# Optimization experiments

Measured on AMD Instinct MI355X. Metric: run time of the kernel, lower is better.

## Reference

```python
import jax, jax.numpy as jnp
import numpy as np

N = 10000        # num_nodes
E = 160000       # num_edges (before self loops)
D_IN = 256       # input_dim
H = 128          # hidden_dim (= per-head out_channels)
HEADS = 4
HD = HEADS * H   # 512
L = 16           # num_layers
OUT = 1024       # output_dim
G = 8            # num graphs in batch
EPS = 1e-5


def _layer_norm(x, w, b):
    m = jnp.mean(x, axis=-1, keepdims=True)
    v = jnp.mean(jnp.square(x - m), axis=-1, keepdims=True)
    return (x - m) / jnp.sqrt(v + EPS) * w + b


def setup_inputs() -> dict:
    key = jax.random.key(0)
    ks = jax.random.split(key, 20)
    s = 0.05
    x = jax.random.normal(ks[0], (N, D_IN), jnp.float32)
    edge_index = jax.random.randint(ks[1], (2, E), 0, N, dtype=jnp.int64)
    batch = jnp.sort(jax.random.randint(ks[2], (N,), 0, G, dtype=jnp.int64))
    return {
        "x": x,
        "edge_index": edge_index,
        "batch": batch,
        "W_in": jax.random.normal(ks[3], (D_IN, H), jnp.float32) * s,
        "b_in": jnp.zeros((H,), jnp.float32),
        "ln_in_w": jnp.ones((H,), jnp.float32),
        "ln_in_b": jnp.zeros((H,), jnp.float32),
        "Wsrc": jax.random.normal(ks[4], (L, H, HD), jnp.float32) * s,
        "Wdst": jax.random.normal(ks[5], (L, H, HD), jnp.float32) * s,
        "att_src": jax.random.normal(ks[6], (L, HEADS, H), jnp.float32) * s,
        "att_dst": jax.random.normal(ks[7], (L, HEADS, H), jnp.float32) * s,
        "Wout": jax.random.normal(ks[8], (L, HD, H), jnp.float32) * s,
        "bout": jnp.zeros((L, H), jnp.float32),
        "ln_w": jnp.ones((L, H), jnp.float32),
        "ln_b": jnp.zeros((L, H), jnp.float32),
        "Wp1": jax.random.normal(ks[9], (H, OUT), jnp.float32) * s,
        "bp1": jnp.zeros((OUT,), jnp.float32),
        "Wp2": jax.random.normal(ks[10], (OUT, OUT), jnp.float32) * s,
        "bp2": jnp.zeros((OUT,), jnp.float32),
    }


def reference(x, edge_index, batch, W_in, b_in, ln_in_w, ln_in_b,
              Wsrc, Wdst, att_src, att_dst, Wout, bout, ln_w, ln_b,
              Wp1, bp1, Wp2, bp2):
    # add self loops once (same edge set every layer)
    loop = jnp.arange(N, dtype=edge_index.dtype)
    e_src = jnp.concatenate([edge_index[0], loop])  # x_j (source)
    e_dst = jnp.concatenate([edge_index[1], loop])  # x_i (target / aggregate index)

    h = jax.nn.relu(_layer_norm(x @ W_in + b_in, ln_in_w, ln_in_b))  # [N, H]

    for l in range(L):
        hs = (h[e_src] @ Wsrc[l]).reshape(-1, HEADS, H)  # [E2, heads, H]
        hd = (h[e_dst] @ Wdst[l]).reshape(-1, HEADS, H)
        a = jnp.sum(hs * att_src[l], axis=-1) + jnp.sum(hd * att_dst[l], axis=-1)  # [E2, heads]
        a = jax.nn.leaky_relu(a, 0.2)
        # NOTE: faithful to source -- softmax over HEADS per edge, not over neighbors
        a = jax.nn.softmax(a, axis=-1)
        msg = (hs * a[..., None]).reshape(-1, HD)  # [E2, HD]
        agg = jax.ops.segment_sum(msg, e_dst, num_segments=N)  # [N, HD]
        out = agg @ Wout[l] + bout[l]
        h = jax.nn.relu(_layer_norm(out + h, ln_w[l], ln_b[l]))  # residual: H == H

    g = jax.ops.segment_max(h, batch, num_segments=G)  # global max pool [G, H]
    g = jax.nn.relu(g @ Wp1 + bp1)
    return g @ Wp2 + bp2  # [G, OUT]
```

## Files before the change

### kernel.cpp

```cpp
#include <hip/hip_runtime.h>
#include <hip/hip_bf16.h>

#define N_NODES 10000
#define E_EDGES 160000
#define E2 (E_EDGES + N_NODES)
#define D_IN 256
#define H 128
#define HEADS 4
#define HD 512
#define L_LAYERS 16
#define OUT_DIM 1024
#define G_GRAPHS 8
#define EPS 1e-5f
#define SPAD 10016

typedef unsigned short ushort_t;
typedef __attribute__((ext_vector_type(8))) short short8;
typedef __attribute__((ext_vector_type(4))) float f32x4;
typedef __attribute__((ext_vector_type(4))) unsigned u32x4;

__device__ __forceinline__ f32x4 mfma16(short8 a, short8 b, f32x4 c) {
    return __builtin_amdgcn_mfma_f32_16x16x32_bf16(a, b, c, 0, 0, 0);
}
__device__ __forceinline__ unsigned short f2b(float f) {
    unsigned u = __float_as_uint(f);
    u += 0x7fffu + ((u >> 16) & 1u);
    return (unsigned short)(u >> 16);
}
__device__ __forceinline__ unsigned pk2(float lo, float hi) {
    __hip_bfloat162 p = __float22bfloat162_rn(make_float2(lo, hi));
    return *(unsigned*)&p;
}

__global__ void k_zero(int* deg, int* cur, unsigned* g) {
    int i = blockIdx.x * blockDim.x + threadIdx.x;
    if (i < N_NODES) { deg[i] = 0; cur[i] = 0; }
    if (i < G_GRAPHS * H) g[i] = 0u;
}

__global__ void k_count(const int* ei, int* deg) {
    int e = blockIdx.x * blockDim.x + threadIdx.x;
    if (e >= E2) return;
    int d = (e < E_EDGES) ? ei[E_EDGES + e] : (e - E_EDGES);
    atomicAdd(&deg[d], 1);
}

__global__ void k_scan(const int* deg, int* rs) {
    __shared__ int s[1024];
    int t = threadIdx.x;
    int base = t * 10;
    int loc[10], run = 0;
    #pragma unroll
    for (int i = 0; i < 10; i++) {
        int idx = base + i;
        int v = (idx < N_NODES) ? deg[idx] : 0;
        loc[i] = run; run += v;
    }
    s[t] = run;
    __syncthreads();
    for (int off = 1; off < 1024; off <<= 1) {
        int xv = (t >= off) ? s[t - off] : 0;
        __syncthreads();
        s[t] += xv;
        __syncthreads();
    }
    int excl = s[t] - run;
    #pragma unroll
    for (int i = 0; i < 10; i++) {
        int idx = base + i;
        if (idx <= N_NODES) rs[idx] = excl + loc[i];
    }
}

__global__ void k_fill(const int* ei, const int* rs, int* cur, int* elist) {
    int e = blockIdx.x * blockDim.x + threadIdx.x;
    if (e >= E2) return;
    int s, d;
    if (e < E_EDGES) { s = ei[e]; d = ei[E_EDGES + e]; }
    else { s = d = e - E_EDGES; }
    int pos = atomicAdd(&cur[d], 1);
    elist[rs[d] + pos] = s;
}

__global__ void k_vw(const float* Wsrc, const float* Wdst,
                     const float* att_src, const float* att_dst,
                     float* vsrc, float* vdst) {
    int l = blockIdx.x;
    int t = threadIdx.x;
    int head = t >> 7, j = t & 127;
    const float* Ws = Wsrc + (size_t)l * H * HD;
    const float* Wd = Wdst + (size_t)l * H * HD;
    const float* As = att_src + (size_t)l * HEADS * H;
    const float* Ad = att_dst + (size_t)l * HEADS * H;
    float ss = 0.f, sd = 0.f;
    for (int k = 0; k < H; k++) {
        ss += Ws[(size_t)j * HD + head * H + k] * As[head * H + k];
        sd += Wd[(size_t)j * HD + head * H + k] * Ad[head * H + k];
    }
    vsrc[(size_t)l * HD + head * H + j] = ss;
    vdst[(size_t)l * HD + head * H + j] = sd;
}

__global__ __launch_bounds__(256) void k_mm(const float* __restrict__ Wsrc,
        const float* __restrict__ Wout, float* __restrict__ M) {
    int bid = blockIdx.x;
    int kq = bid & 3, h = (bid >> 2) & 3, l = bid >> 4;
    int t = threadIdx.x;
    int o = t & 127, kh = t >> 7;
    const float* Ws = Wsrc + (size_t)l * H * HD + h * 128;
    const float* Wo = Wout + (size_t)l * HD * H + (size_t)h * 128 * H;
    for (int r = 0; r < 16; r++) {
        int k = kq * 32 + kh * 16 + r;
        float acc = 0.f;
        for (int c = 0; c < 128; c++)
            acc += Ws[(size_t)k * HD + c] * Wo[(size_t)c * H + o];
        M[(size_t)l * HD * H + (size_t)(h * 128 + k) * H + o] = acc;
    }
}

__global__ void k_pack_out(const float* W, ushort_t* Wp) {
    int idx = blockIdx.x * 256 + threadIdx.x;
    int l = idx >> 16, rem = idx & 65535;
    int k = rem >> 7, col = rem & 127;
    float v = W[(size_t)l * HD * H + (size_t)k * H + col];
    int nt = col >> 4, ks = k >> 5, lhi = (k >> 3) & 3, llo = col & 15, j = k & 7;
    Wp[(size_t)l * 65536 + (((size_t)(nt * 16 + ks) * 64) + lhi * 16 + llo) * 8 + j] = f2b(v);
}

__global__ void k_pack_win(const float* W, ushort_t* Wp) {
    int idx = blockIdx.x * 256 + threadIdx.x;
    int k = idx >> 7, col = idx & 127;
    float v = W[(size_t)k * H + col];
    int nt = col >> 4, ks = k >> 5, lhi = (k >> 3) & 3, llo = col & 15, j = k & 7;
    Wp[(((size_t)(nt * 8 + ks) * 64) + lhi * 16 + llo) * 8 + j] = f2b(v);
}

__global__ __launch_bounds__(256) void k_in_mfma(
        const float* __restrict__ x, const ushort_t* __restrict__ WpI,
        const float* __restrict__ b_in, const float* __restrict__ lnw,
        const float* __restrict__ lnb, float* __restrict__ h, ushort_t* __restrict__ hb) {
    __shared__ float part1[4][16], part2[4][16];
    int t = threadIdx.x, w = t >> 6, lane = t & 63;
    int row0 = blockIdx.x * 16;
    int ar = lane & 15, ac = (lane >> 4) * 8;
    short8 a[8];
    #pragma unroll
    for (int ks = 0; ks < 8; ks++) {
        const float* xp = x + (size_t)(row0 + ar) * D_IN + ks * 32 + ac;
        float4 xa = *(const float4*)xp;
        float4 xb = *(const float4*)(xp + 4);
        u32x4 u;
        u.x = pk2(xa.x, xa.y); u.y = pk2(xa.z, xa.w);
        u.z = pk2(xb.x, xb.y); u.w = pk2(xb.z, xb.w);
        a[ks] = *(short8*)&u;
    }
    const ushort_t* B0 = WpI + ((size_t)(w * 2 + 0) * 8) * 64 * 8;
    const ushort_t* B1 = WpI + ((size_t)(w * 2 + 1) * 8) * 64 * 8;
    f32x4 c0 = {0.f, 0.f, 0.f, 0.f}, c1 = {0.f, 0.f, 0.f, 0.f};
    #pragma unroll
    for (int ks = 0; ks < 8; ks++) {
        short8 b0 = *(const short8*)(B0 + ((size_t)ks * 64 + lane) * 8);
        short8 b1 = *(const short8*)(B1 + ((size_t)ks * 64 + lane) * 8);
        c0 = mfma16(a[ks], b0, c0);
        c1 = mfma16(a[ks], b1, c1);
    }
    int col0 = (w * 2 + 0) * 16 + ar, col1 = (w * 2 + 1) * 16 + ar;
    int rb = (lane >> 4) * 4;
    float v0[4], v1[4];
    #pragma unroll
    for (int r = 0; r < 4; r++) {
        v0[r] = c0[r] + b_in[col0];
        v1[r] = c1[r] + b_in[col1];
        float p1 = v0[r] + v1[r];
        float p2 = v0[r] * v0[r] + v1[r] * v1[r];
        #pragma unroll
        for (int off = 1; off < 16; off <<= 1) {
            p1 += __shfl_xor(p1, off);
            p2 += __shfl_xor(p2, off);
        }
        if (ar == 0) { part1[w][rb + r] = p1; part2[w][rb + r] = p2; }
    }
    __syncthreads();
    #pragma unroll
    for (int r = 0; r < 4; r++) {
        int lr = rb + r;
        int row = row0 + lr;
        float s1 = part1[0][lr] + part1[1][lr] + part1[2][lr] + part1[3][lr];
        float s2 = part2[0][lr] + part2[1][lr] + part2[2][lr] + part2[3][lr];
        float m = s1 * (1.f / 128.f);
        float var = s2 * (1.f / 128.f) - m * m;
        float is = rsqrtf(var + EPS);
        float y0 = fmaxf((v0[r] - m) * is * lnw[col0] + lnb[col0], 0.f);
        float y1 = fmaxf((v1[r] - m) * is * lnw[col1] + lnb[col1], 0.f);
        h[(size_t)row * H + col0] = y0;
        h[(size_t)row * H + col1] = y1;
        hb[(size_t)row * H + col0] = f2b(y0);
        hb[(size_t)row * H + col1] = f2b(y1);
    }
}

__global__ __launch_bounds__(256) void k_alpha(const float* __restrict__ h,
        const float* __restrict__ vsrc, const float* __restrict__ vdst,
        float* __restrict__ as_, float* __restrict__ ad_, int l) {
    int wid = threadIdx.x >> 6, lane = threadIdx.x & 63;
    int n = blockIdx.x * 4 + wid;
    float h0 = h[(size_t)n * H + lane];
    float h1 = h[(size_t)n * H + 64 + lane];
    const float* vs = vsrc + (size_t)l * HD;
    const float* vd = vdst + (size_t)l * HD;
    #pragma unroll
    for (int d = 0; d < HEADS; d++) {
        float p = h0 * vs[d * H + lane] + h1 * vs[d * H + 64 + lane];
        float q = h0 * vd[d * H + lane] + h1 * vd[d * H + 64 + lane];
        #pragma unroll
        for (int off = 32; off > 0; off >>= 1) {
            p += __shfl_down(p, off);
            q += __shfl_down(q, off);
        }
        if (lane == 0) { as_[n * HEADS + d] = p; ad_[n * HEADS + d] = q; }
    }
}

#define ACC1(uv, wt) do { \
    acc[0] += (wt) * __uint_as_float((uv).x << 16); \
    acc[1] += (wt) * __uint_as_float((uv).x & 0xffff0000u); \
    acc[2] += (wt) * __uint_as_float((uv).y << 16); \
    acc[3] += (wt) * __uint_as_float((uv).y & 0xffff0000u); \
    acc[4] += (wt) * __uint_as_float((uv).z << 16); \
    acc[5] += (wt) * __uint_as_float((uv).z & 0xffff0000u); \
    acc[6] += (wt) * __uint_as_float((uv).w << 16); \
    acc[7] += (wt) * __uint_as_float((uv).w & 0xffff0000u); \
} while (0)

__global__ __launch_bounds__(256) void k_aggout(
        const ushort_t* __restrict__ hb, const float4* __restrict__ as4,
        const float4* __restrict__ ad4, const int* __restrict__ rs,
        const int* __restrict__ elist, const ushort_t* __restrict__ Wp,
        const float* __restrict__ bout, const float* __restrict__ lnw,
        const float* __restrict__ lnb, float* __restrict__ h,
        ushort_t* __restrict__ hbo, int l) {
    __shared__ ushort_t frag[16 * 64 * 8];
    __shared__ int sl[4][64];
    __shared__ float wl[4][64][4];
    __shared__ float part1[4][16], part2[4][16];
    int t = threadIdx.x, w = t >> 6, lane = t & 63;
    int base = blockIdx.x * 16;
    int head = lane >> 4;
    int j8 = (lane & 15) * 8;

    for (int q = 0; q < 4; q++) {
        int r = w * 4 + q;
        int node = base + r;
        int start = rs[node], end = rs[node + 1];
        float4 adv = ad4[node];
        float acc[8];
        #pragma unroll
        for (int i = 0; i < 8; i++) acc[i] = 0.f;
        for (int c0 = start; c0 < end; c0 += 64) {
            int cnt = min(64, end - c0);
            if (lane < cnt) {
                int s = elist[c0 + lane];
                sl[w][lane] = s;
                float4 av = as4[s];
                float l0 = av.x + adv.x, l1 = av.y + adv.y, l2 = av.z + adv.z, l3 = av.w + adv.w;
                l0 = (l0 > 0.f) ? l0 : 0.2f * l0;
                l1 = (l1 > 0.f) ? l1 : 0.2f * l1;
                l2 = (l2 > 0.f) ? l2 : 0.2f * l2;
                l3 = (l3 > 0.f) ? l3 : 0.2f * l3;
                float mx = fmaxf(fmaxf(l0, l1), fmaxf(l2, l3));
                float e0 = expf(l0 - mx), e1 = expf(l1 - mx), e2 = expf(l2 - mx), e3 = expf(l3 - mx);
                float inv = 1.f / (e0 + e1 + e2 + e3);
                wl[w][lane][0] = e0 * inv;
                wl[w][lane][1] = e1 * inv;
                wl[w][lane][2] = e2 * inv;
                wl[w][lane][3] = e3 * inv;
            }
            __asm__ volatile("s_waitcnt lgkmcnt(0)" ::: "memory");
            int j = 0;
            if (cnt >= 4) {
                u32x4 b0, b1, b2, b3;
                float q0, q1, q2, q3;
                {
                    int s0 = sl[w][0], s1 = sl[w][1], s2 = sl[w][2], s3 = sl[w][3];
                    q0 = wl[w][0][head]; q1 = wl[w][1][head];
                    q2 = wl[w][2][head]; q3 = wl[w][3][head];
                    b0 = *(const u32x4*)(hb + (size_t)s0 * H + j8);
                    b1 = *(const u32x4*)(hb + (size_t)s1 * H + j8);
                    b2 = *(const u32x4*)(hb + (size_t)s2 * H + j8);
                    b3 = *(const u32x4*)(hb + (size_t)s3 * H + j8);
                }
                for (j = 4; j + 3 < cnt; j += 4) {
                    int s0 = sl[w][j], s1 = sl[w][j + 1], s2 = sl[w][j + 2], s3 = sl[w][j + 3];
                    u32x4 n0 = *(const u32x4*)(hb + (size_t)s0 * H + j8);
                    u32x4 n1 = *(const u32x4*)(hb + (size_t)s1 * H + j8);
                    u32x4 n2 = *(const u32x4*)(hb + (size_t)s2 * H + j8);
                    u32x4 n3 = *(const u32x4*)(hb + (size_t)s3 * H + j8);
                    float r0 = wl[w][j][head], r1 = wl[w][j + 1][head];
                    float r2 = wl[w][j + 2][head], r3 = wl[w][j + 3][head];
                    ACC1(b0, q0); ACC1(b1, q1); ACC1(b2, q2); ACC1(b3, q3);
                    b0 = n0; q0 = r0; b1 = n1; q1 = r1;
                    b2 = n2; q2 = r2; b3 = n3; q3 = r3;
                }
                ACC1(b0, q0); ACC1(b1, q1); ACC1(b2, q2); ACC1(b3, q3);
            }
            for (; j < cnt; j++) {
                int s = sl[w][j];
                float wt = wl[w][j][head];
                u32x4 uv = *(const u32x4*)(hb + (size_t)s * H + j8);
                ACC1(uv, wt);
            }
        }
        u32x4 o;
        o.x = pk2(acc[0], acc[1]);
        o.y = pk2(acc[2], acc[3]);
        o.z = pk2(acc[4], acc[5]);
        o.w = pk2(acc[6], acc[7]);
        int ksn = head * 4 + ((lane >> 2) & 3);
        int gidx = ((lane & 3) * 16 + r) * 16 + (ksn ^ r);
        *(u32x4*)((char*)frag + gidx * 16) = o;
    }
    __syncthreads();

    const ushort_t* WL = Wp + (size_t)l * 65536;
    short8 a[16];
    #pragma unroll
    for (int ks = 0; ks < 16; ks++) {
        int gidx = lane * 16 + (ks ^ (lane & 15));
        a[ks] = *(const short8*)((const char*)frag + gidx * 16);
    }
    int ar = lane & 15;
    f32x4 c0 = {0.f, 0.f, 0.f, 0.f}, c1 = {0.f, 0.f, 0.f, 0.f};
    #pragma unroll
    for (int ks = 0; ks < 16; ks++) {
        short8 b0 = *(const short8*)(WL + ((size_t)((w * 2 + 0) * 16 + ks) * 64 + lane) * 8);
        short8 b1 = *(const short8*)(WL + ((size_t)((w * 2 + 1) * 16 + ks) * 64 + lane) * 8);
        c0 = mfma16(a[ks], b0, c0);
        c1 = mfma16(a[ks], b1, c1);
    }

    const float* bo = bout + (size_t)l * H;
    const float* gw = lnw + (size_t)l * H;
    const float* gb = lnb + (size_t)l * H;
    int col0 = (w * 2 + 0) * 16 + ar;
    int col1 = (w * 2 + 1) * 16 + ar;
    int rb = (lane >> 4) * 4;
    float v0[4], v1[4];
    #pragma unroll
    for (int r = 0; r < 4; r++) {
        int row = base + rb + r;
        v0[r] = c0[r] + bo[col0] + h[(size_t)row * H + col0];
        v1[r] = c1[r] + bo[col1] + h[(size_t)row * H + col1];
        float p1 = v0[r] + v1[r];
        float p2 = v0[r] * v0[r] + v1[r] * v1[r];
        #pragma unroll
        for (int off = 1; off < 16; off <<= 1) {
            p1 += __shfl_xor(p1, off);
            p2 += __shfl_xor(p2, off);
        }
        if (ar == 0) { part1[w][rb + r] = p1; part2[w][rb + r] = p2; }
    }
    __syncthreads();
    #pragma unroll
    for (int r = 0; r < 4; r++) {
        int lr = rb + r;
        int row = base + lr;
        float s1 = part1[0][lr] + part1[1][lr] + part1[2][lr] + part1[3][lr];
        float s2 = part2[0][lr] + part2[1][lr] + part2[2][lr] + part2[3][lr];
        float m = s1 * (1.f / 128.f);
        float var = s2 * (1.f / 128.f) - m * m;
        float is = rsqrtf(var + EPS);
        float y0 = fmaxf((v0[r] - m) * is * gw[col0] + gb[col0], 0.f);
        float y1 = fmaxf((v1[r] - m) * is * gw[col1] + gb[col1], 0.f);
        h[(size_t)row * H + col0] = y0;
        h[(size_t)row * H + col1] = y1;
        hbo[(size_t)row * H + col0] = f2b(y0);
        hbo[(size_t)row * H + col1] = f2b(y1);
    }
}

__global__ void k_pool(const float* __restrict__ h, const int* __restrict__ batch,
                       unsigned* __restrict__ g) {
    __shared__ float lm[G_GRAPHS][H];
    int t = threadIdx.x;
    #pragma unroll
    for (int i = 0; i < G_GRAPHS; i++) lm[i][t] = 0.f;
    int n0 = blockIdx.x * 100, n1 = n0 + 100;
    for (int n = n0; n < n1; n++) {
        int b = batch[n];
        lm[b][t] = fmaxf(lm[b][t], h[(size_t)n * H + t]);
    }
    #pragma unroll
    for (int i = 0; i < G_GRAPHS; i++)
        atomicMax(&g[i * H + t], __float_as_uint(lm[i][t]));
}

__global__ void k_mlp1(const unsigned* __restrict__ g, const float* __restrict__ Wp1,
                       const float* __restrict__ bp1, float* __restrict__ g1) {
    __shared__ float gs[H];
    int gr = blockIdx.x >> 2, ch = blockIdx.x & 3;
    int t = threadIdx.x;
    if (t < H) gs[t] = __uint_as_float(g[gr * H + t]);
    __syncthreads();
    int col = ch * 256 + t;
    float acc = 0.f;
    for (int k = 0; k < H; k++) acc += gs[k] * Wp1[(size_t)k * OUT_DIM + col];
    acc += bp1[col];
    g1[(size_t)gr * OUT_DIM + col] = fmaxf(acc, 0.f);
}

__global__ void k_mlp2(const float* __restrict__ g1, const float* __restrict__ Wp2,
                       const float* __restrict__ bp2, float* __restrict__ out) {
    __shared__ float gs[OUT_DIM];
    __shared__ float part[4][64];
    int gr = blockIdx.x >> 4, ch = blockIdx.x & 15;
    int t = threadIdx.x;
    int ci = t & 63, si = t >> 6;
    for (int i = t; i < OUT_DIM; i += 256) gs[i] = g1[(size_t)gr * OUT_DIM + i];
    __syncthreads();
    int col = ch * 64 + ci;
    float acc = 0.f;
    for (int k = si * 256; k < si * 256 + 256; k++)
        acc += gs[k] * Wp2[(size_t)k * OUT_DIM + col];
    part[si][ci] = acc;
    __syncthreads();
    if (si == 0) {
        float r = part[0][ci] + part[1][ci] + part[2][ci] + part[3][ci] + bp2[col];
        out[(size_t)gr * OUT_DIM + col] = r;
    }
}

extern "C" void kernel_launch(void* const* d_in, const int* in_sizes, int n_in,
                              void* d_out, int out_size, void* d_ws, size_t ws_size,
                              hipStream_t stream) {
    const float* x       = (const float*)d_in[0];
    const int*   ei      = (const int*)d_in[1];
    const int*   batch   = (const int*)d_in[2];
    const float* W_in    = (const float*)d_in[3];
    const float* b_in    = (const float*)d_in[4];
    const float* ln_in_w = (const float*)d_in[5];
    const float* ln_in_b = (const float*)d_in[6];
    const float* Wsrc    = (const float*)d_in[7];
    const float* Wdst    = (const float*)d_in[8];
    const float* att_src = (const float*)d_in[9];
    const float* att_dst = (const float*)d_in[10];
    const float* Wout    = (const float*)d_in[11];
    const float* bout    = (const float*)d_in[12];
    const float* ln_w    = (const float*)d_in[13];
    const float* ln_b    = (const float*)d_in[14];
    const float* Wp1     = (const float*)d_in[15];
    const float* bp1     = (const float*)d_in[16];
    const float* Wp2     = (const float*)d_in[17];
    const float* bp2     = (const float*)d_in[18];

    char* w = (char*)d_ws;
    auto alloc = [&](size_t bytes) { void* p = w; w += (bytes + 255) & ~(size_t)255; return p; };
    float*     h     = (float*)alloc((size_t)N_NODES * H * 4);
    ushort_t*  hb    = (ushort_t*)alloc((size_t)SPAD * H * 2);
    float*     as_   = (float*)alloc((size_t)SPAD * HEADS * 4);
    float*     ad_   = (float*)alloc((size_t)SPAD * HEADS * 4);
    float*     vsrc  = (float*)alloc((size_t)L_LAYERS * HD * 4);
    float*     vdst  = (float*)alloc((size_t)L_LAYERS * HD * 4);
    float*     M     = (float*)alloc((size_t)L_LAYERS * HD * H * 4);
    ushort_t*  WpM   = (ushort_t*)alloc((size_t)L_LAYERS * 65536 * 2);
    ushort_t*  WpI   = (ushort_t*)alloc((size_t)D_IN * H * 2);
    int*       deg   = (int*)alloc((size_t)N_NODES * 4);
    int*       rs    = (int*)alloc((size_t)(N_NODES + 1) * 4);
    int*       cur   = (int*)alloc((size_t)N_NODES * 4);
    int*       elist = (int*)alloc((size_t)E2 * 4);
    unsigned*  g     = (unsigned*)alloc((size_t)G_GRAPHS * H * 4);
    float*     g1    = (float*)alloc((size_t)G_GRAPHS * OUT_DIM * 4);

    k_zero<<<40, 256, 0, stream>>>(deg, cur, g);
    k_count<<<(E2 + 255) / 256, 256, 0, stream>>>(ei, deg);
    k_scan<<<1, 1024, 0, stream>>>(deg, rs);
    k_fill<<<(E2 + 255) / 256, 256, 0, stream>>>(ei, rs, cur, elist);
    k_vw<<<L_LAYERS, 512, 0, stream>>>(Wsrc, Wdst, att_src, att_dst, vsrc, vdst);
    k_mm<<<256, 256, 0, stream>>>(Wsrc, Wout, M);
    k_pack_out<<<4096, 256, 0, stream>>>(M, WpM);
    k_pack_win<<<128, 256, 0, stream>>>(W_in, WpI);
    k_in_mfma<<<N_NODES / 16, 256, 0, stream>>>(x, WpI, b_in, ln_in_w, ln_in_b, h, hb);

    for (int l = 0; l < L_LAYERS; l++) {
        k_alpha<<<N_NODES / 4, 256, 0, stream>>>(h, vsrc, vdst, as_, ad_, l);
        k_aggout<<<N_NODES / 16, 256, 0, stream>>>(hb, (const float4*)as_, (const float4*)ad_,
                                                   rs, elist, WpM, bout, ln_w, ln_b, h, hb, l);
    }

    k_pool<<<100, 128, 0, stream>>>(h, batch, g);
    k_mlp1<<<G_GRAPHS * 4, 256, 0, stream>>>(g, Wp1, bp1, g1);
    k_mlp2<<<G_GRAPHS * 16, 256, 0, stream>>>(g1, Wp2, bp2, (float*)d_out);
}
```

Measured before the change: 719.8 us.

## Fuse attention-logit computation into layer epilogue, split weights hi/lo, widen aggout

Removes the per-layer k_alpha launch by computing next-layer source/destination attention dot products inside the k_aggout epilogue (and the first layer's inside k_in_mfma), with ping-pong buffers for hb and alpha to avoid read/write races. The fused weight matrix is now stored as bf16 high plus bf16 residual parts and applied with twice the MFMAs for better precision. k_aggout moves to 512 threads with one 16-column tile per wave, and the weight-product precompute kernel uses shared-memory tiling. This saves sixteen launches and a read of h per layer, at the cost of extra MFMA work and a larger block.

```diff
diff --git a/kernel.cpp b/kernel.cpp
--- a/kernel.cpp
+++ b/kernel.cpp
@@ -26,6 +26,9 @@
     unsigned u = __float_as_uint(f);
     u += 0x7fffu + ((u >> 16) & 1u);
     return (unsigned short)(u >> 16);
+}
+__device__ __forceinline__ float b2f(unsigned short b) {
+    return __uint_as_float((unsigned)b << 16);
 }
 __device__ __forceinline__ unsigned pk2(float lo, float hi) {
     __hip_bfloat162 p = __float22bfloat162_rn(make_float2(lo, hi));
@@ -103,28 +106,68 @@
 
 __global__ __launch_bounds__(256) void k_mm(const float* __restrict__ Wsrc,
         const float* __restrict__ Wout, float* __restrict__ M) {
+    __shared__ float As[32][33];
+    __shared__ float Bs[32][128];
     int bid = blockIdx.x;
-    int kq = bid & 3, h = (bid >> 2) & 3, l = bid >> 4;
+    int q = bid & 3, hh = (bid >> 2) & 3, l = bid >> 4;
     int t = threadIdx.x;
-    int o = t & 127, kh = t >> 7;
-    const float* Ws = Wsrc + (size_t)l * H * HD + h * 128;
-    const float* Wo = Wout + (size_t)l * HD * H + (size_t)h * 128 * H;
-    for (int r = 0; r < 16; r++) {
-        int k = kq * 32 + kh * 16 + r;
-        float acc = 0.f;
-        for (int c = 0; c < 128; c++)
-            acc += Ws[(size_t)k * HD + c] * Wo[(size_t)c * H + o];
-        M[(size_t)l * HD * H + (size_t)(h * 128 + k) * H + o] = acc;
-    }
-}
-
-__global__ void k_pack_out(const float* W, ushort_t* Wp) {
+    int ty = t >> 4, tx = t & 15;
+    const float* WsB = Wsrc + (size_t)l * H * HD + (size_t)hh * 128;
+    const float* WoB = Wout + (size_t)l * HD * H + (size_t)hh * 128 * H;
+    float acc[2][8];
+    #pragma unroll
+    for (int r = 0; r < 2; r++)
+        #pragma unroll
+        for (int c = 0; c < 8; c++) acc[r][c] = 0.f;
+    for (int kt = 0; kt < 4; kt++) {
+        #pragma unroll
+        for (int i = 0; i < 4; i++) {
+            int lin = i * 256 + t;
+            int rr = lin >> 5, cc = lin & 31;
+            As[rr][cc] = WsB[(size_t)(q * 32 + rr) * HD + kt * 32 + cc];
+        }
+        #pragma unroll
+        for (int i = 0; i < 16; i++) {
+            int lin = i * 256 + t;
+            int rr = lin >> 7, cc = lin & 127;
+            Bs[rr][cc] = WoB[(size_t)(kt * 32 + rr) * H + cc];
+        }
+        __syncthreads();
+        #pragma unroll
+        for (int kk = 0; kk < 32; kk++) {
+            float a0 = As[ty * 2][kk], a1 = As[ty * 2 + 1][kk];
+            float4 b0 = *(const float4*)&Bs[kk][tx * 8];
+            float4 b1 = *(const float4*)&Bs[kk][tx * 8 + 4];
+            acc[0][0] += a0 * b0.x; acc[0][1] += a0 * b0.y;
+            acc[0][2] += a0 * b0.z; acc[0][3] += a0 * b0.w;
+            acc[0][4] += a0 * b1.x; acc[0][5] += a0 * b1.y;
+            acc[0][6] += a0 * b1.z; acc[0][7] += a0 * b1.w;
+            acc[1][0] += a1 * b0.x; acc[1][1] += a1 * b0.y;
+            acc[1][2] += a1 * b0.z; acc[1][3] += a1 * b0.w;
+            acc[1][4] += a1 * b1.x; acc[1][5] += a1 * b1.y;
+            acc[1][6] += a1 * b1.z; acc[1][7] += a1 * b1.w;
+        }
+        __syncthreads();
+    }
+    #pragma unroll
+    for (int r = 0; r < 2; r++)
+        #pragma unroll
+        for (int c = 0; c < 8; c++)
+            M[(size_t)l * HD * H + (size_t)(hh * 128 + q * 32 + ty * 2 + r) * H + tx * 8 + c]
+                = acc[r][c];
+}
+
+__global__ void k_pack_out2(const float* M, ushort_t* Wh, ushort_t* Wl) {
     int idx = blockIdx.x * 256 + threadIdx.x;
     int l = idx >> 16, rem = idx & 65535;
     int k = rem >> 7, col = rem & 127;
-    float v = W[(size_t)l * HD * H + (size_t)k * H + col];
+    float v = M[(size_t)l * HD * H + (size_t)k * H + col];
+    unsigned short hi = f2b(v);
+    unsigned short lo = f2b(v - b2f(hi));
     int nt = col >> 4, ks = k >> 5, lhi = (k >> 3) & 3, llo = col & 15, j = k & 7;
-    Wp[(size_t)l * 65536 + (((size_t)(nt * 16 + ks) * 64) + lhi * 16 + llo) * 8 + j] = f2b(v);
+    size_t addr = (size_t)l * 65536 + (((size_t)(nt * 16 + ks) * 64) + lhi * 16 + llo) * 8 + j;
+    Wh[addr] = hi;
+    Wl[addr] = lo;
 }
 
 __global__ void k_pack_win(const float* W, ushort_t* Wp) {
@@ -138,8 +181,11 @@
 __global__ __launch_bounds__(256) void k_in_mfma(
         const float* __restrict__ x, const ushort_t* __restrict__ WpI,
         const float* __restrict__ b_in, const float* __restrict__ lnw,
-        const float* __restrict__ lnb, float* __restrict__ h, ushort_t* __restrict__ hb) {
+        const float* __restrict__ lnb, const float* __restrict__ vs,
+        const float* __restrict__ vd, float* __restrict__ as0, float* __restrict__ ad0,
+        float* __restrict__ h, ushort_t* __restrict__ hb) {
     __shared__ float part1[4][16], part2[4][16];
+    __shared__ float apart[4][8][16];
     int t = threadIdx.x, w = t >> 6, lane = t & 63;
     int row0 = blockIdx.x * 16;
     int ar = lane & 15, ac = (lane >> 4) * 8;
@@ -164,9 +210,9 @@
         c0 = mfma16(a[ks], b0, c0);
         c1 = mfma16(a[ks], b1, c1);
     }
-    int col0 = (w * 2 + 0) * 16 + ar, col1 = (w * 2 + 1) * 16 + ar;
+    int col0 = w * 32 + ar, col1 = w * 32 + 16 + ar;
     int rb = (lane >> 4) * 4;
-    float v0[4], v1[4];
+    float v0[4], v1[4], y0[4], y1[4];
     #pragma unroll
     for (int r = 0; r < 4; r++) {
         v0[r] = c0[r] + b_in[col0];
@@ -190,34 +236,36 @@
         float m = s1 * (1.f / 128.f);
         float var = s2 * (1.f / 128.f) - m * m;
         float is = rsqrtf(var + EPS);
-        float y0 = fmaxf((v0[r] - m) * is * lnw[col0] + lnb[col0], 0.f);
-        float y1 = fmaxf((v1[r] - m) * is * lnw[col1] + lnb[col1], 0.f);
-        h[(size_t)row * H + col0] = y0;
-        h[(size_t)row * H + col1] = y1;
-        hb[(size_t)row * H + col0] = f2b(y0);
-        hb[(size_t)row * H + col1] = f2b(y1);
-    }
-}
-
-__global__ __launch_bounds__(256) void k_alpha(const float* __restrict__ h,
-        const float* __restrict__ vsrc, const float* __restrict__ vdst,
-        float* __restrict__ as_, float* __restrict__ ad_, int l) {
-    int wid = threadIdx.x >> 6, lane = threadIdx.x & 63;
-    int n = blockIdx.x * 4 + wid;
-    float h0 = h[(size_t)n * H + lane];
-    float h1 = h[(size_t)n * H + 64 + lane];
-    const float* vs = vsrc + (size_t)l * HD;
-    const float* vd = vdst + (size_t)l * HD;
-    #pragma unroll
-    for (int d = 0; d < HEADS; d++) {
-        float p = h0 * vs[d * H + lane] + h1 * vs[d * H + 64 + lane];
-        float q = h0 * vd[d * H + lane] + h1 * vd[d * H + 64 + lane];
-        #pragma unroll
-        for (int off = 32; off > 0; off >>= 1) {
-            p += __shfl_down(p, off);
-            q += __shfl_down(q, off);
-        }
-        if (lane == 0) { as_[n * HEADS + d] = p; ad_[n * HEADS + d] = q; }
+        y0[r] = fmaxf((v0[r] - m) * is * lnw[col0] + lnb[col0], 0.f);
+        y1[r] = fmaxf((v1[r] - m) * is * lnw[col1] + lnb[col1], 0.f);
+        h[(size_t)row * H + col0] = y0[r];
+        h[(size_t)row * H + col1] = y1[r];
+        hb[(size_t)row * H + col0] = f2b(y0[r]);
+        hb[(size_t)row * H + col1] = f2b(y1[r]);
+    }
+    #pragma unroll
+    for (int comp = 0; comp < 8; comp++) {
+        float vc0 = (comp < 4) ? vs[comp * H + col0] : vd[(comp - 4) * H + col0];
+        float vc1 = (comp < 4) ? vs[comp * H + col1] : vd[(comp - 4) * H + col1];
+        float p[4];
+        #pragma unroll
+        for (int r = 0; r < 4; r++) p[r] = y0[r] * vc0 + y1[r] * vc1;
+        #pragma unroll
+        for (int off = 1; off < 16; off <<= 1)
+            #pragma unroll
+            for (int r = 0; r < 4; r++) p[r] += __shfl_xor(p[r], off);
+        if (ar == 0)
+            #pragma unroll
+            for (int r = 0; r < 4; r++) apart[w][comp][rb + r] = p[r];
+    }
+    __syncthreads();
+    if (t < 128) {
+        int lr = t >> 3, comp = t & 7;
+        float s = apart[0][comp][lr] + apart[1][comp][lr]
+                + apart[2][comp][lr] + apart[3][comp][lr];
+        int node = row0 + lr;
+        if (comp < 4) as0[node * 4 + comp] = s;
+        else          ad0[node * 4 + comp - 4] = s;
     }
 }
 
@@ -232,24 +280,27 @@
     acc[7] += (wt) * __uint_as_float((uv).w & 0xffff0000u); \
 } while (0)
 
-__global__ __launch_bounds__(256) void k_aggout(
+__global__ __launch_bounds__(512) void k_aggout(
         const ushort_t* __restrict__ hb, const float4* __restrict__ as4,
         const float4* __restrict__ ad4, const int* __restrict__ rs,
-        const int* __restrict__ elist, const ushort_t* __restrict__ Wp,
-        const float* __restrict__ bout, const float* __restrict__ lnw,
-        const float* __restrict__ lnb, float* __restrict__ h,
-        ushort_t* __restrict__ hbo, int l) {
+        const int* __restrict__ elist, const ushort_t* __restrict__ Wh,
+        const ushort_t* __restrict__ Wl, const float* __restrict__ bout,
+        const float* __restrict__ lnw, const float* __restrict__ lnb,
+        const float* __restrict__ vsn, const float* __restrict__ vdn,
+        float* __restrict__ asn, float* __restrict__ adn, int doAlpha,
+        float* __restrict__ h, ushort_t* __restrict__ hbo, int l) {
     __shared__ ushort_t frag[16 * 64 * 8];
-    __shared__ int sl[4][64];
-    __shared__ float wl[4][64][4];
-    __shared__ float part1[4][16], part2[4][16];
+    __shared__ int sl[8][64];
+    __shared__ float wl[8][64][4];
+    __shared__ float part1[8][16], part2[8][16];
+    __shared__ float apart[8][8][16];
     int t = threadIdx.x, w = t >> 6, lane = t & 63;
     int base = blockIdx.x * 16;
     int head = lane >> 4;
     int j8 = (lane & 15) * 8;
 
-    for (int q = 0; q < 4; q++) {
-        int r = w * 4 + q;
+    for (int q = 0; q < 2; q++) {
+        int r = w * 2 + q;
         int node = base + r;
         int start = rs[node], end = rs[node + 1];
         float4 adv = ad4[node];
@@ -321,7 +372,8 @@
     }
     __syncthreads();
 
-    const ushort_t* WL = Wp + (size_t)l * 65536;
+    const ushort_t* WLh = Wh + (size_t)l * 65536;
+    const ushort_t* WLl = Wl + (size_t)l * 65536;
     short8 a[16];
     #pragma unroll
     for (int ks = 0; ks < 16; ks++) {
@@ -329,29 +381,30 @@
         a[ks] = *(const short8*)((const char*)frag + gidx * 16);
     }
     int ar = lane & 15;
-    f32x4 c0 = {0.f, 0.f, 0.f, 0.f}, c1 = {0.f, 0.f, 0.f, 0.f};
+    f32x4 c = {0.f, 0.f, 0.f, 0.f};
     #pragma unroll
     for (int ks = 0; ks < 16; ks++) {
-        short8 b0 = *(const short8*)(WL + ((size_t)((w * 2 + 0) * 16 + ks) * 64 + lane) * 8);
-        short8 b1 = *(const short8*)(WL + ((size_t)((w * 2 + 1) * 16 + ks) * 64 + lane) * 8);
-        c0 = mfma16(a[ks], b0, c0);
-        c1 = mfma16(a[ks], b1, c1);
+        short8 bh = *(const short8*)(WLh + ((size_t)(w * 16 + ks) * 64 + lane) * 8);
+        c = mfma16(a[ks], bh, c);
+    }
+    #pragma unroll
+    for (int ks = 0; ks < 16; ks++) {
+        short8 bl = *(const short8*)(WLl + ((size_t)(w * 16 + ks) * 64 + lane) * 8);
+        c = mfma16(a[ks], bl, c);
     }
 
     const float* bo = bout + (size_t)l * H;
     const float* gw = lnw + (size_t)l * H;
     const float* gb = lnb + (size_t)l * H;
-    int col0 = (w * 2 + 0) * 16 + ar;
-    int col1 = (w * 2 + 1) * 16 + ar;
+    int col = w * 16 + ar;
     int rb = (lane >> 4) * 4;
-    float v0[4], v1[4];
+    float v[4], y[4];
     #pragma unroll
     for (int r = 0; r < 4; r++) {
         int row = base + rb + r;
-        v0[r] = c0[r] + bo[col0] + h[(size_t)row * H + col0];
-        v1[r] = c1[r] + bo[col1] + h[(size_t)row * H + col1];
-        float p1 = v0[r] + v1[r];
-        float p2 = v0[r] * v0[r] + v1[r] * v1[r];
+        v[r] = c[r] + bo[col] + h[(size_t)row * H + col];
+        float p1 = v[r];
+        float p2 = v[r] * v[r];
         #pragma unroll
         for (int off = 1; off < 16; off <<= 1) {
             p1 += __shfl_xor(p1, off);
@@ -364,17 +417,42 @@
     for (int r = 0; r < 4; r++) {
         int lr = rb + r;
         int row = base + lr;
-        float s1 = part1[0][lr] + part1[1][lr] + part1[2][lr] + part1[3][lr];
-        float s2 = part2[0][lr] + part2[1][lr] + part2[2][lr] + part2[3][lr];
+        float s1 = 0.f, s2 = 0.f;
+        #pragma unroll
+        for (int ww = 0; ww < 8; ww++) { s1 += part1[ww][lr]; s2 += part2[ww][lr]; }
         float m = s1 * (1.f / 128.f);
         float var = s2 * (1.f / 128.f) - m * m;
         float is = rsqrtf(var + EPS);
-        float y0 = fmaxf((v0[r] - m) * is * gw[col0] + gb[col0], 0.f);
-        float y1 = fmaxf((v1[r] - m) * is * gw[col1] + gb[col1], 0.f);
-        h[(size_t)row * H + col0] = y0;
-        h[(size_t)row * H + col1] = y1;
-        hbo[(size_t)row * H + col0] = f2b(y0);
-        hbo[(size_t)row * H + col1] = f2b(y1);
+        y[r] = fmaxf((v[r] - m) * is * gw[col] + gb[col], 0.f);
+        h[(size_t)row * H + col] = y[r];
+        hbo[(size_t)row * H + col] = f2b(y[r]);
+    }
+
+    if (doAlpha) {
+        #pragma unroll
+        for (int comp = 0; comp < 8; comp++) {
+            float vc = (comp < 4) ? vsn[comp * H + col] : vdn[(comp - 4) * H + col];
+            float p[4];
+            #pragma unroll
+            for (int r = 0; r < 4; r++) p[r] = y[r] * vc;
+            #pragma unroll
+            for (int off = 1; off < 16; off <<= 1)
+                #pragma unroll
+                for (int r = 0; r < 4; r++) p[r] += __shfl_xor(p[r], off);
+            if (ar == 0)
+                #pragma unroll
+                for (int r = 0; r < 4; r++) apart[w][comp][rb + r] = p[r];
+        }
+        __syncthreads();
+        if (t < 128) {
+            int lr = t >> 3, comp = t & 7;
+            float s = 0.f;
+            #pragma unroll
+            for (int ww = 0; ww < 8; ww++) s += apart[ww][comp][lr];
+            int node = base + lr;
+            if (comp < 4) asn[node * 4 + comp] = s;
+            else          adn[node * 4 + comp - 4] = s;
+        }
     }
 }
 
@@ -455,13 +533,17 @@
     char* w = (char*)d_ws;
     auto alloc = [&](size_t bytes) { void* p = w; w += (bytes + 255) & ~(size_t)255; return p; };
     float*     h     = (float*)alloc((size_t)N_NODES * H * 4);
-    ushort_t*  hb    = (ushort_t*)alloc((size_t)SPAD * H * 2);
-    float*     as_   = (float*)alloc((size_t)SPAD * HEADS * 4);
-    float*     ad_   = (float*)alloc((size_t)SPAD * HEADS * 4);
+    ushort_t*  hb0   = (ushort_t*)alloc((size_t)SPAD * H * 2);
+    ushort_t*  hb1   = (ushort_t*)alloc((size_t)SPAD * H * 2);
+    float*     as0   = (float*)alloc((size_t)SPAD * HEADS * 4);
+    float*     ad0   = (float*)alloc((size_t)SPAD * HEADS * 4);
+    float*     as1   = (float*)alloc((size_t)SPAD * HEADS * 4);
+    float*     ad1   = (float*)alloc((size_t)SPAD * HEADS * 4);
     float*     vsrc  = (float*)alloc((size_t)L_LAYERS * HD * 4);
     float*     vdst  = (float*)alloc((size_t)L_LAYERS * HD * 4);
     float*     M     = (float*)alloc((size_t)L_LAYERS * HD * H * 4);
-    ushort_t*  WpM   = (ushort_t*)alloc((size_t)L_LAYERS * 65536 * 2);
+    ushort_t*  WpH   = (ushort_t*)alloc((size_t)L_LAYERS * 65536 * 2);
+    ushort_t*  WpL   = (ushort_t*)alloc((size_t)L_LAYERS * 65536 * 2);
     ushort_t*  WpI   = (ushort_t*)alloc((size_t)D_IN * H * 2);
     int*       deg   = (int*)alloc((size_t)N_NODES * 4);
     int*       rs    = (int*)alloc((size_t)(N_NODES + 1) * 4);
@@ -476,14 +558,23 @@
     k_fill<<<(E2 + 255) / 256, 256, 0, stream>>>(ei, rs, cur, elist);
     k_vw<<<L_LAYERS, 512, 0, stream>>>(Wsrc, Wdst, att_src, att_dst, vsrc, vdst);
     k_mm<<<256, 256, 0, stream>>>(Wsrc, Wout, M);
-    k_pack_out<<<4096, 256, 0, stream>>>(M, WpM);
+    k_pack_out2<<<4096, 256, 0, stream>>>(M, WpH, WpL);
     k_pack_win<<<128, 256, 0, stream>>>(W_in, WpI);
-    k_in_mfma<<<N_NODES / 16, 256, 0, stream>>>(x, WpI, b_in, ln_in_w, ln_in_b, h, hb);
+    k_in_mfma<<<N_NODES / 16, 256, 0, stream>>>(x, WpI, b_in, ln_in_w, ln_in_b,
+                                                vsrc, vdst, as0, ad0, h, hb0);
 
     for (int l = 0; l < L_LAYERS; l++) {
-        k_alpha<<<N_NODES / 4, 256, 0, stream>>>(h, vsrc, vdst, as_, ad_, l);
-        k_aggout<<<N_NODES / 16, 256, 0, stream>>>(hb, (const float4*)as_, (const float4*)ad_,
-                                                   rs, elist, WpM, bout, ln_w, ln_b, h, hb, l);
+        const ushort_t* hbi = (l & 1) ? hb1 : hb0;
+        ushort_t*       hbo = (l & 1) ? hb0 : hb1;
+        const float* aA = (l & 1) ? as1 : as0;
+        const float* dA = (l & 1) ? ad1 : ad0;
+        float* aB = (l & 1) ? as0 : as1;
+        float* dB = (l & 1) ? ad0 : ad1;
+        int ln = (l + 1 < L_LAYERS) ? (l + 1) : (L_LAYERS - 1);
+        k_aggout<<<N_NODES / 16, 512, 0, stream>>>(
+            hbi, (const float4*)aA, (const float4*)dA, rs, elist, WpH, WpL,
+            bout, ln_w, ln_b, vsrc + (size_t)ln * HD, vdst + (size_t)ln * HD,
+            aB, dB, (l + 1 < L_LAYERS) ? 1 : 0, h, hbo, l);
     }
 
     k_pool<<<100, 128, 0, stream>>>(h, batch, g);
```

After: 708.0 us. No clear change (-1.6%).
